# Optimization experiments

Measured on AMD Instinct MI355X. Metric: run time of the kernel, lower is better.

The kernel has to match this reference:

```python
import jax, jax.numpy as jnp
import numpy as np

B, L, E = 2, 8192, 1024
H, D = 16, 64          # num_heads, head_dim (E = H*D)
C = 256                # chunk_size
EPS = 1e-6
LN_EPS = 1e-5


def setup_inputs() -> dict:
    key = jax.random.key(0)
    ks = jax.random.split(key, 12)
    w = lambda k, shape: (jax.random.normal(k, shape, jnp.float32) * 0.02)
    return {
        "x": jax.random.normal(ks[0], (B, L, E), jnp.float32),
        "Wq": w(ks[1], (E, E)), "bq": jnp.zeros((E,), jnp.float32),
        "Wk": w(ks[2], (E, E)), "bk": jnp.zeros((E,), jnp.float32),
        "Wv": w(ks[3], (E, E)), "bv": jnp.zeros((E,), jnp.float32),
        "Wo": w(ks[4], (E, E)), "bo": jnp.zeros((E,), jnp.float32),
        "gamma": jnp.ones((E,), jnp.float32),
        "beta": jnp.zeros((E,), jnp.float32),
    }


def _split_heads(t):
    # [B, L, E] -> [B, H, L, D]
    return t.reshape(B, L, H, D).transpose(0, 2, 1, 3)


def _phi(x):
    # feature map: elu(x) + 1  (strictly positive)
    return jax.nn.elu(x) + 1.0


def _chunkwise_linear_attention(q, k, v):
    """Causal linear attention via chunkwise parallel scan.

    q, k, v: [B, H, L, D] (q, k already feature-mapped, positive).
    out[t] = q_t @ S_t / (q_t . z_t), S_t = sum_{s<=t} k_s v_s^T, z_t = sum_{s<=t} k_s.
    """
    N = L // C
    # [N, B, H, C, D]
    qc = q.reshape(B, H, N, C, D).transpose(2, 0, 1, 3, 4)
    kc = k.reshape(B, H, N, C, D).transpose(2, 0, 1, 3, 4)
    vc = v.reshape(B, H, N, C, D).transpose(2, 0, 1, 3, 4)
    mask = jnp.tril(jnp.ones((C, C), q.dtype))  # causal within chunk (inclusive)

    def step(carry, inp):
        S, z = carry                      # S: [B,H,D,D], z: [B,H,D]
        qi, ki, vi = inp                  # [B,H,C,D]
        scores = jnp.einsum("bhcd,bhed->bhce", qi, ki) * mask  # [B,H,C,C]
        num = jnp.einsum("bhcd,bhde->bhce", qi, S) \
            + jnp.einsum("bhce,bhed->bhcd", scores, vi)
        den = jnp.einsum("bhcd,bhd->bhc", qi, z) + scores.sum(-1)
        out = num / (den + EPS)[..., None]
        S = S + jnp.einsum("bhcd,bhce->bhde", ki, vi)
        z = z + ki.sum(axis=2)
        return (S, z), out

    S0 = jnp.zeros((B, H, D, D), q.dtype)
    z0 = jnp.zeros((B, H, D), q.dtype)
    _, outs = jax.lax.scan(step, (S0, z0), (qc, kc, vc))
    # [N,B,H,C,D] -> [B,H,L,D]
    return outs.transpose(1, 2, 0, 3, 4).reshape(B, H, L, D)


def _layer_norm(x, gamma, beta):
    mu = x.mean(-1, keepdims=True)
    var = ((x - mu) ** 2).mean(-1, keepdims=True)
    return gamma * (x - mu) * jax.lax.rsqrt(var + LN_EPS) + beta


def reference(x, Wq, bq, Wk, bk, Wv, bv, Wo, bo, gamma, beta):
    residual = x
    q = _phi(_split_heads(x @ Wq + bq))
    k = _phi(_split_heads(x @ Wk + bk))
    v = _split_heads(x @ Wv + bv)
    out = _chunkwise_linear_attention(q, k, v)      # [B,H,L,D]
    out = out.transpose(0, 2, 1, 3).reshape(B, L, E)
    out = out @ Wo + bo
    return _layer_norm(out + residual, gamma, beta)
```

## Files before the change

### kernel.cpp

```cpp
#include <hip/hip_runtime.h>
#include <stdint.h>

typedef __attribute__((ext_vector_type(8))) short bf16x8;
typedef __attribute__((ext_vector_type(4))) float f32x4;
typedef __attribute__((ext_vector_type(2))) unsigned int u32x2;
typedef unsigned short u16;
typedef unsigned int u32;

#define MFMA16(a, b, c) __builtin_amdgcn_mfma_f32_16x16x32_bf16((a), (b), (c), 0, 0, 0)

__device__ __forceinline__ u16 f2bf(float f) {
  union { float f; u32 u; } c; c.f = f;
  u32 u = c.u;
  return (u16)((u + 0x7FFFu + ((u >> 16) & 1u)) >> 16);
}

__device__ __forceinline__ float bf2f(u16 h) {
  union { u32 u; float f; } c;
  c.u = ((u32)h) << 16;
  return c.f;
}

__device__ __forceinline__ void gll16(const void* g, void* l) {
  __builtin_amdgcn_global_load_lds((__attribute__((address_space(1))) void*)(g),
                                   (__attribute__((address_space(3))) void*)(l),
                                   16, 0, 0);
}

__global__ __launch_bounds__(256) void cast_k(const float* __restrict__ x, u16* __restrict__ xb) {
  int idx = blockIdx.x * 256 + threadIdx.x;
#pragma unroll
  for (int it = 0; it < 4; it++) {
    size_t i = (size_t)idx + (size_t)it * 1048576;
    float4 v = ((const float4*)x)[i];
    u32x2 p;
    p.x = (u32)f2bf(v.x) | ((u32)f2bf(v.y) << 16);
    p.y = (u32)f2bf(v.z) | ((u32)f2bf(v.w) << 16);
    ((u32x2*)xb)[i] = p;
  }
}

__global__ __launch_bounds__(256) void wT_k(const float* __restrict__ Wq, const float* __restrict__ Wk,
                                            const float* __restrict__ Wv, const float* __restrict__ Wo,
                                            u16* __restrict__ wqkvT, u16* __restrict__ woT) {
  __shared__ float t[32][33];
  int which = blockIdx.z;
  const float* W = (which == 0) ? Wq : (which == 1) ? Wk : (which == 2) ? Wv : Wo;
  int k0 = blockIdx.y * 32, n0 = blockIdx.x * 32;
  int c = threadIdx.x & 31, r8 = threadIdx.x >> 5;
#pragma unroll
  for (int rr = 0; rr < 32; rr += 8)
    t[r8 + rr][c] = W[(size_t)(k0 + r8 + rr) * 1024 + n0 + c];
  __syncthreads();
  u16* outp = (which < 3) ? (wqkvT + (size_t)which * 1048576) : woT;
#pragma unroll
  for (int rr = 0; rr < 32; rr += 8)
    outp[(size_t)(n0 + r8 + rr) * 1024 + k0 + c] = f2bf(t[c][r8 + rr]);
}

template <int MODE>
__global__ __launch_bounds__(256, 2) void gemm_k(
    const u16* __restrict__ A, const u16* __restrict__ Bt,
    const float* __restrict__ b0, const float* __restrict__ b1, const float* __restrict__ b2,
    u16* __restrict__ q_o, u16* __restrict__ k_o, u16* __restrict__ vt_o,
    const u16* __restrict__ xres, u16* __restrict__ y_o) {
  __shared__ u16 As[2][4096];
  __shared__ u16 Bs[2][4096];
  const int tid = threadIdx.x;
  const int wave = tid >> 6, lane = tid & 63;
  const int quad = lane >> 4, l16 = lane & 15;
  const int wr = wave >> 1, wc = wave & 1;
  const int bm = blockIdx.x, bn = blockIdx.y;

  const int r_a = wave * 32 + (lane >> 2);
  const int c_a = (lane & 3) * 8;
  const size_t arow = (size_t)bm * 128;
  const size_t brow = (size_t)bn * 128;

  f32x4 zero = {0.f, 0.f, 0.f, 0.f};
  f32x4 acc[4][4];
#pragma unroll
  for (int i = 0; i < 4; i++)
#pragma unroll
    for (int j = 0; j < 4; j++) acc[i][j] = zero;

  for (int k0 = 0; k0 < 1024; k0 += 64) {
#pragma unroll
    for (int h = 0; h < 2; h++) {
      const int kk = k0 + h * 32;
#pragma unroll
      for (int jc = 0; jc < 2; jc++) {
        int r = r_a + jc * 16;
        int lo = wave * 1024 + jc * 512 + lane * 8;
        gll16(A + (arow + r) * 1024 + kk + c_a, &As[h][lo]);
        gll16(Bt + (brow + r) * 1024 + kk + c_a, &Bs[h][lo]);
      }
    }
    __syncthreads();
#pragma unroll
    for (int h = 0; h < 2; h++) {
      bf16x8 af[4], bf[4];
#pragma unroll
      for (int t = 0; t < 4; t++) af[t] = *(const bf16x8*)&As[h][(wr * 64 + t * 16 + l16) * 32 + quad * 8];
#pragma unroll
      for (int t = 0; t < 4; t++) bf[t] = *(const bf16x8*)&Bs[h][(wc * 64 + t * 16 + l16) * 32 + quad * 8];
#pragma unroll
      for (int i = 0; i < 4; i++)
#pragma unroll
        for (int j = 0; j < 4; j++) acc[i][j] = MFMA16(af[i], bf[j], acc[i][j]);
    }
    __syncthreads();
  }

  if (MODE == 0) {
#pragma unroll
    for (int i = 0; i < 4; i++) {
      const int m0 = bm * 128 + wr * 64 + i * 16 + quad * 4;
      const int b = m0 >> 13, l0 = m0 & 8191;
      const int nch = l0 >> 8, c0 = l0 & 255;
#pragma unroll
      for (int j = 0; j < 4; j++) {
        const int n_g = bn * 128 + wc * 64 + j * 16 + l16;
        const int sec = n_g >> 10, e = n_g & 1023;
        const float* bias = (sec == 0) ? b0 : ((sec == 1) ? b1 : b2);
        const float be = bias[e];
        float v4[4];
#pragma unroll
        for (int r = 0; r < 4; r++) {
          float v = acc[i][j][r] + be;
          if (sec < 2) v = (v > 0.f) ? (v + 1.f) : __expf(v);
          v4[r] = v;
        }
        const int h = e >> 6, d = e & 63;
        const int bh = b * 16 + h;
        if (sec == 2) {
          u32x2 p;
          p.x = (u32)f2bf(v4[0]) | ((u32)f2bf(v4[1]) << 16);
          p.y = (u32)f2bf(v4[2]) | ((u32)f2bf(v4[3]) << 16);
          *(u32x2*)&vt_o[(((size_t)(bh * 32 + nch)) * 64 + d) * 256 + c0] = p;
        } else {
          u16* dst = (sec == 0) ? q_o : k_o;
          const size_t tb = (((size_t)bh * 8192 + l0) << 6) + d;
#pragma unroll
          for (int r = 0; r < 4; r++) dst[tb + (size_t)r * 64] = f2bf(v4[r]);
        }
      }
    }
  } else {
#pragma unroll
    for (int i = 0; i < 4; i++) {
#pragma unroll
      for (int j = 0; j < 4; j++) {
#pragma unroll
        for (int r = 0; r < 4; r++) {
          int m_g = bm * 128 + wr * 64 + i * 16 + quad * 4 + r;
          int n_g = bn * 128 + wc * 64 + j * 16 + l16;
          float v = acc[i][j][r] + b0[n_g] + bf2f(xres[(size_t)m_g * 1024 + n_g]);
          y_o[(size_t)m_g * 1024 + n_g] = f2bf(v);
        }
      }
    }
  }
}

__global__ __launch_bounds__(256, 2) void phaseA_k(const u16* __restrict__ kb, const u16* __restrict__ vt,
                                                   float* __restrict__ ST, float* __restrict__ zc) {
  __shared__ u16 kT[64 * 264];
  const int tid = threadIdx.x;
  const int wave = tid >> 6, lane = tid & 63;
  const int quad = lane >> 4, l16 = lane & 15;
  const int wr = wave >> 1, wc = wave & 1;
  const int bhn = blockIdx.x;
  const u16* kc = kb + (size_t)bhn * 16384;
  const u16* vtc = vt + (size_t)bhn * 16384;

#pragma unroll
  for (int t = 0; t < 2; t++) {
    const int dblk = wave + 4 * t;
#pragma unroll
    for (int itc = 0; itc < 4; itc++) {
      const int c = itc * 64 + lane;
      bf16x8 kv = *(const bf16x8*)&kc[c * 64 + dblk * 8];
#pragma unroll
      for (int j = 0; j < 8; j++) kT[(dblk * 8 + j) * 264 + c] = (u16)kv[j];
    }
  }
  __syncthreads();

  f32x4 zero = {0.f, 0.f, 0.f, 0.f};
  f32x4 t4[2][2];
  f32x4 za[2];
#pragma unroll
  for (int i = 0; i < 2; i++) {
    za[i] = zero;
#pragma unroll
    for (int j = 0; j < 2; j++) t4[i][j] = zero;
  }
  bf16x8 ones;
#pragma unroll
  for (int j = 0; j < 8; j++) ones[j] = (short)0x3F80;

#pragma unroll
  for (int ks = 0; ks < 8; ks++) {
    bf16x8 av[2], bk2[2];
#pragma unroll
    for (int t = 0; t < 2; t++) av[t] = *(const bf16x8*)&vtc[(wr * 32 + t * 16 + l16) * 256 + ks * 32 + quad * 8];
#pragma unroll
    for (int t = 0; t < 2; t++) bk2[t] = *(const bf16x8*)&kT[(wc * 32 + t * 16 + l16) * 264 + ks * 32 + quad * 8];
#pragma unroll
    for (int i = 0; i < 2; i++)
#pragma unroll
      for (int j = 0; j < 2; j++) t4[i][j] = MFMA16(av[i], bk2[j], t4[i][j]);
    if (wr == 0) {
#pragma unroll
      for (int j = 0; j < 2; j++) za[j] = MFMA16(ones, bk2[j], za[j]);
    }
  }
  float* Sg = ST + (size_t)bhn * 4096;
#pragma unroll
  for (int i = 0; i < 2; i++)
#pragma unroll
    for (int j = 0; j < 2; j++)
#pragma unroll
      for (int r = 0; r < 4; r++)
        Sg[(wr * 32 + i * 16 + quad * 4 + r) * 64 + wc * 32 + j * 16 + l16] = t4[i][j][r];
  if (wr == 0 && quad == 0) {
#pragma unroll
    for (int j = 0; j < 2; j++) zc[(size_t)bhn * 64 + wc * 32 + j * 16 + l16] = za[j][0];
  }
}

__global__ __launch_bounds__(256) void phaseB_k(const float* __restrict__ ST, const float* __restrict__ zc,
                                                u16* __restrict__ STp, u16* __restrict__ zp) {
  const int blk = blockIdx.x, tid = threadIdx.x;
  if (blk < 512) {
    const int bh = blk >> 4;
    const int e = ((blk & 15) << 8) + tid;
    const size_t base = (size_t)bh * 32 * 4096 + e;
    float run = 0.f;
#pragma unroll
    for (int n = 0; n < 32; n++) {
      float v = ST[base + (size_t)n * 4096];
      STp[base + (size_t)n * 4096] = f2bf(run);
      run += v;
    }
  } else {
    const int idx = (blk - 512) * 256 + tid;
    const int bh = idx >> 6, d = idx & 63;
    const size_t zb = (size_t)bh * 2048 + d;
    float run = 0.f;
#pragma unroll
    for (int n = 0; n < 32; n++) {
      float v = zc[zb + n * 64];
      zp[zb + n * 64] = f2bf(run);
      run += v;
    }
  }
}

__global__ __launch_bounds__(256, 2) void phaseC_k(const u16* __restrict__ qb, const u16* __restrict__ kb,
                                                   const u16* __restrict__ vt, const u16* __restrict__ STp,
                                                   const u16* __restrict__ zp, u16* __restrict__ ao) {
  __shared__ u16 P[4][64 * 72];
  const int tid = threadIdx.x;
  const int wave = tid >> 6, lane = tid & 63;
  const int quad = lane >> 4, l16 = lane & 15;
  const int bhn = blockIdx.x;
  const int bh = bhn >> 5, n = bhn & 31;
  const int b = bh >> 4, h = bh & 15;
  const size_t cbase = (size_t)bhn * 16384;
  const u16* qc = qb + cbase;
  const u16* kc = kb + cbase;
  const u16* vtc = vt + cbase;
  const u16* STg = STp + (size_t)bhn * 4096;
  const u16* zg = zp + (size_t)bhn * 64;

  f32x4 zero = {0.f, 0.f, 0.f, 0.f};
  f32x4 num[4][4];
  f32x4 den[4];
#pragma unroll
  for (int i = 0; i < 4; i++) {
    den[i] = zero;
#pragma unroll
    for (int j = 0; j < 4; j++) num[i][j] = zero;
  }
  bf16x8 ones;
#pragma unroll
  for (int j = 0; j < 8; j++) ones[j] = (short)0x3F80;

  bf16x8 aq[4][2];
#pragma unroll
  for (int i = 0; i < 4; i++)
#pragma unroll
    for (int ks = 0; ks < 2; ks++)
      aq[i][ks] = *(const bf16x8*)&qc[(wave * 64 + i * 16 + l16) * 64 + ks * 32 + quad * 8];

#pragma unroll
  for (int ks = 0; ks < 2; ks++) {
    bf16x8 bz = *(const bf16x8*)&zg[ks * 32 + quad * 8];
    bf16x8 bs[4];
#pragma unroll
    for (int j = 0; j < 4; j++) bs[j] = *(const bf16x8*)&STg[(j * 16 + l16) * 64 + ks * 32 + quad * 8];
#pragma unroll
    for (int i = 0; i < 4; i++) {
      den[i] = MFMA16(aq[i][ks], bz, den[i]);
#pragma unroll
      for (int j = 0; j < 4; j++) num[i][j] = MFMA16(aq[i][ks], bs[j], num[i][j]);
    }
  }

  u16* Pw = &P[wave][0];

  for (int cc = 0; cc <= wave; cc++) {
    bf16x8 bkf[2][4];
#pragma unroll
    for (int ks = 0; ks < 2; ks++)
#pragma unroll
      for (int j = 0; j < 4; j++)
        bkf[ks][j] = *(const bf16x8*)&kc[(cc * 64 + j * 16 + l16) * 64 + ks * 32 + quad * 8];
#pragma unroll
    for (int i = 0; i < 4; i++) {
      f32x4 sc4[4];
#pragma unroll
      for (int j = 0; j < 4; j++) sc4[j] = zero;
#pragma unroll
      for (int ks = 0; ks < 2; ks++)
#pragma unroll
        for (int j = 0; j < 4; j++) sc4[j] = MFMA16(aq[i][ks], bkf[ks][j], sc4[j]);
#pragma unroll
      for (int j = 0; j < 4; j++) {
#pragma unroll
        for (int r = 0; r < 4; r++) {
          int row = wave * 64 + i * 16 + quad * 4 + r;
          int col = cc * 64 + j * 16 + l16;
          float v = (col <= row) ? sc4[j][r] : 0.f;
          Pw[(i * 16 + quad * 4 + r) * 72 + j * 16 + l16] = f2bf(v);
        }
      }
    }
    bf16x8 bvf[2][4];
#pragma unroll
    for (int ks2 = 0; ks2 < 2; ks2++)
#pragma unroll
      for (int j = 0; j < 4; j++)
        bvf[ks2][j] = *(const bf16x8*)&vtc[(j * 16 + l16) * 256 + cc * 64 + ks2 * 32 + quad * 8];
#pragma unroll
    for (int i = 0; i < 4; i++) {
#pragma unroll
      for (int ks2 = 0; ks2 < 2; ks2++) {
        bf16x8 ap = *(const bf16x8*)&Pw[(i * 16 + l16) * 72 + ks2 * 32 + quad * 8];
#pragma unroll
        for (int j = 0; j < 4; j++) num[i][j] = MFMA16(ap, bvf[ks2][j], num[i][j]);
        den[i] = MFMA16(ap, ones, den[i]);
      }
    }
  }

#pragma unroll
  for (int i = 0; i < 4; i++)
#pragma unroll
    for (int j = 0; j < 4; j++)
#pragma unroll
      for (int r = 0; r < 4; r++) {
        int row = wave * 64 + i * 16 + quad * 4 + r;
        int col = j * 16 + l16;
        float o = num[i][j][r] / (den[i][r] + 1e-6f);
        int l = n * 256 + row;
        ao[(((size_t)b * 8192 + l) * 16 + h) * 64 + col] = f2bf(o);
      }
}

__global__ __launch_bounds__(256) void ln_k(const u16* __restrict__ y, const float* __restrict__ gamma,
                                            const float* __restrict__ beta, float* __restrict__ o) {
  int row = blockIdx.x, tid = threadIdx.x;
  u32x2 pv = ((const u32x2*)(y + (size_t)row * 1024))[tid];
  float vx = bf2f((u16)(pv.x & 0xFFFF)), vy = bf2f((u16)(pv.x >> 16));
  float vz = bf2f((u16)(pv.y & 0xFFFF)), vw = bf2f((u16)(pv.y >> 16));
  float s = vx + vy + vz + vw;
  float s2 = vx * vx + vy * vy + vz * vz + vw * vw;
#pragma unroll
  for (int off = 32; off; off >>= 1) {
    s += __shfl_down(s, off, 64);
    s2 += __shfl_down(s2, off, 64);
  }
  __shared__ float red[8];
  int wave = tid >> 6, lane = tid & 63;
  if (lane == 0) { red[wave] = s; red[4 + wave] = s2; }
  __syncthreads();
  s = red[0] + red[1] + red[2] + red[3];
  s2 = red[4] + red[5] + red[6] + red[7];
  float mu = s * 0.0009765625f;
  float var = s2 * 0.0009765625f - mu * mu;
  float inv = rsqrtf(var + 1e-5f);
  float4 g = ((const float4*)gamma)[tid];
  float4 bb = ((const float4*)beta)[tid];
  float4 ov;
  ov.x = g.x * (vx - mu) * inv + bb.x;
  ov.y = g.y * (vy - mu) * inv + bb.y;
  ov.z = g.z * (vz - mu) * inv + bb.z;
  ov.w = g.w * (vw - mu) * inv + bb.w;
  ((float4*)(o + (size_t)row * 1024))[tid] = ov;
}

extern "C" void kernel_launch(void* const* d_in, const int* in_sizes, int n_in,
                              void* d_out, int out_size, void* d_ws, size_t ws_size,
                              hipStream_t stream) {
  const float* x = (const float*)d_in[0];
  const float* Wq = (const float*)d_in[1];
  const float* bq = (const float*)d_in[2];
  const float* Wk = (const float*)d_in[3];
  const float* bk = (const float*)d_in[4];
  const float* Wv = (const float*)d_in[5];
  const float* bv = (const float*)d_in[6];
  const float* Wo = (const float*)d_in[7];
  const float* bo = (const float*)d_in[8];
  const float* gamma = (const float*)d_in[9];
  const float* beta = (const float*)d_in[10];

  char* ws = (char*)d_ws;
  u16* xb = (u16*)(ws + 0);
  u16* qb = (u16*)(ws + 33554432);
  u16* kb = (u16*)(ws + 67108864);
  u16* attno = (u16*)(ws + 100663296);
  u16* vt = (u16*)(ws + 134217728);
  u16* wqkvT = (u16*)(ws + 167772160);
  u16* woT = (u16*)(ws + 174063616);
  float* SchT = (float*)(ws + 176160768);
  float* zch = (float*)(ws + 192937984);
  u16* STp = (u16*)(ws + 193200128);
  u16* zp = (u16*)(ws + 201588736);
  u16* ypre = qb;

  cast_k<<<4096, 256, 0, stream>>>(x, xb);
  wT_k<<<dim3(32, 32, 4), 256, 0, stream>>>(Wq, Wk, Wv, Wo, wqkvT, woT);
  gemm_k<0><<<dim3(128, 24), 256, 0, stream>>>(xb, wqkvT, bq, bk, bv, qb, kb, vt, nullptr, nullptr);
  phaseA_k<<<1024, 256, 0, stream>>>(kb, vt, SchT, zch);
  phaseB_k<<<520, 256, 0, stream>>>(SchT, zch, STp, zp);
  phaseC_k<<<1024, 256, 0, stream>>>(qb, kb, vt, STp, zp, attno);
  gemm_k<1><<<dim3(128, 8), 256, 0, stream>>>(attno, woT, bo, nullptr, nullptr, nullptr, nullptr, nullptr, xb,
                                              ypre);
  ln_k<<<16384, 256, 0, stream>>>(ypre, gamma, beta, (float*)d_out);
}
```

Baseline: 389.4 us.

## Merge prep kernels, swap GEMM grid order, store chunk states in bf16

```diff
diff --git a/kernel.cpp b/kernel.cpp
--- a/kernel.cpp
+++ b/kernel.cpp
@@ -27,39 +27,42 @@
                                    16, 0, 0);
 }
 
-__global__ __launch_bounds__(256) void cast_k(const float* __restrict__ x, u16* __restrict__ xb) {
-  int idx = blockIdx.x * 256 + threadIdx.x;
-#pragma unroll
-  for (int it = 0; it < 4; it++) {
-    size_t i = (size_t)idx + (size_t)it * 1048576;
-    float4 v = ((const float4*)x)[i];
-    u32x2 p;
-    p.x = (u32)f2bf(v.x) | ((u32)f2bf(v.y) << 16);
-    p.y = (u32)f2bf(v.z) | ((u32)f2bf(v.w) << 16);
-    ((u32x2*)xb)[i] = p;
-  }
-}
-
-__global__ __launch_bounds__(256) void wT_k(const float* __restrict__ Wq, const float* __restrict__ Wk,
-                                            const float* __restrict__ Wv, const float* __restrict__ Wo,
-                                            u16* __restrict__ wqkvT, u16* __restrict__ woT) {
-  __shared__ float t[32][33];
-  int which = blockIdx.z;
-  const float* W = (which == 0) ? Wq : (which == 1) ? Wk : (which == 2) ? Wv : Wo;
-  int k0 = blockIdx.y * 32, n0 = blockIdx.x * 32;
-  int c = threadIdx.x & 31, r8 = threadIdx.x >> 5;
-#pragma unroll
-  for (int rr = 0; rr < 32; rr += 8)
-    t[r8 + rr][c] = W[(size_t)(k0 + r8 + rr) * 1024 + n0 + c];
-  __syncthreads();
-  u16* outp = (which < 3) ? (wqkvT + (size_t)which * 1048576) : woT;
-#pragma unroll
-  for (int rr = 0; rr < 32; rr += 8)
-    outp[(size_t)(n0 + r8 + rr) * 1024 + k0 + c] = f2bf(t[c][r8 + rr]);
+__global__ __launch_bounds__(256) void prep_k(const float* __restrict__ x, u16* __restrict__ xb,
+                                              const float* __restrict__ Wq, const float* __restrict__ Wk,
+                                              const float* __restrict__ Wv, const float* __restrict__ Wo,
+                                              u16* __restrict__ wqkvT, u16* __restrict__ woT) {
+  const int blk = blockIdx.x;
+  if (blk < 4096) {
+    int idx = blk * 256 + threadIdx.x;
+#pragma unroll
+    for (int it = 0; it < 4; it++) {
+      size_t i = (size_t)idx + (size_t)it * 1048576;
+      float4 v = ((const float4*)x)[i];
+      u32x2 p;
+      p.x = (u32)f2bf(v.x) | ((u32)f2bf(v.y) << 16);
+      p.y = (u32)f2bf(v.z) | ((u32)f2bf(v.w) << 16);
+      ((u32x2*)xb)[i] = p;
+    }
+  } else {
+    __shared__ float t[32][33];
+    const int id = blk - 4096;
+    const int which = id >> 10, rem = id & 1023;
+    const float* W = (which == 0) ? Wq : (which == 1) ? Wk : (which == 2) ? Wv : Wo;
+    int k0 = (rem >> 5) * 32, n0 = (rem & 31) * 32;
+    int c = threadIdx.x & 31, r8 = threadIdx.x >> 5;
+#pragma unroll
+    for (int rr = 0; rr < 32; rr += 8)
+      t[r8 + rr][c] = W[(size_t)(k0 + r8 + rr) * 1024 + n0 + c];
+    __syncthreads();
+    u16* outp = (which < 3) ? (wqkvT + (size_t)which * 1048576) : woT;
+#pragma unroll
+    for (int rr = 0; rr < 32; rr += 8)
+      outp[(size_t)(n0 + r8 + rr) * 1024 + k0 + c] = f2bf(t[c][r8 + rr]);
+  }
 }
 
 template <int MODE>
-__global__ __launch_bounds__(256, 2) void gemm_k(
+__global__ __launch_bounds__(256, 4) void gemm_k(
     const u16* __restrict__ A, const u16* __restrict__ Bt,
     const float* __restrict__ b0, const float* __restrict__ b1, const float* __restrict__ b2,
     u16* __restrict__ q_o, u16* __restrict__ k_o, u16* __restrict__ vt_o,
@@ -70,7 +73,7 @@
   const int wave = tid >> 6, lane = tid & 63;
   const int quad = lane >> 4, l16 = lane & 15;
   const int wr = wave >> 1, wc = wave & 1;
-  const int bm = blockIdx.x, bn = blockIdx.y;
+  const int bn = blockIdx.x, bm = blockIdx.y;
 
   const int r_a = wave * 32 + (lane >> 2);
   const int c_a = (lane & 3) * 8;
@@ -164,7 +167,7 @@
 }
 
 __global__ __launch_bounds__(256, 2) void phaseA_k(const u16* __restrict__ kb, const u16* __restrict__ vt,
-                                                   float* __restrict__ ST, float* __restrict__ zc) {
+                                                   u16* __restrict__ Sch, u16* __restrict__ zc) {
   __shared__ u16 kT[64 * 264];
   const int tid = threadIdx.x;
   const int wave = tid >> 6, lane = tid & 63;
@@ -216,21 +219,21 @@
       for (int j = 0; j < 2; j++) za[j] = MFMA16(ones, bk2[j], za[j]);
     }
   }
-  float* Sg = ST + (size_t)bhn * 4096;
+  u16* Sg = Sch + (size_t)bhn * 4096;
 #pragma unroll
   for (int i = 0; i < 2; i++)
 #pragma unroll
     for (int j = 0; j < 2; j++)
 #pragma unroll
       for (int r = 0; r < 4; r++)
-        Sg[(wr * 32 + i * 16 + quad * 4 + r) * 64 + wc * 32 + j * 16 + l16] = t4[i][j][r];
+        Sg[(wr * 32 + i * 16 + quad * 4 + r) * 64 + wc * 32 + j * 16 + l16] = f2bf(t4[i][j][r]);
   if (wr == 0 && quad == 0) {
 #pragma unroll
-    for (int j = 0; j < 2; j++) zc[(size_t)bhn * 64 + wc * 32 + j * 16 + l16] = za[j][0];
-  }
-}
-
-__global__ __launch_bounds__(256) void phaseB_k(const float* __restrict__ ST, const float* __restrict__ zc,
+    for (int j = 0; j < 2; j++) zc[(size_t)bhn * 64 + wc * 32 + j * 16 + l16] = f2bf(za[j][0]);
+  }
+}
+
+__global__ __launch_bounds__(256) void phaseB_k(const u16* __restrict__ Sch, const u16* __restrict__ zc,
                                                 u16* __restrict__ STp, u16* __restrict__ zp) {
   const int blk = blockIdx.x, tid = threadIdx.x;
   if (blk < 512) {
@@ -240,7 +243,7 @@
     float run = 0.f;
 #pragma unroll
     for (int n = 0; n < 32; n++) {
-      float v = ST[base + (size_t)n * 4096];
+      float v = bf2f(Sch[base + (size_t)n * 4096]);
       STp[base + (size_t)n * 4096] = f2bf(run);
       run += v;
     }
@@ -251,7 +254,7 @@
     float run = 0.f;
 #pragma unroll
     for (int n = 0; n < 32; n++) {
-      float v = zc[zb + n * 64];
+      float v = bf2f(zc[zb + n * 64]);
       zp[zb + n * 64] = f2bf(run);
       run += v;
     }
@@ -425,19 +428,18 @@
   u16* vt = (u16*)(ws + 134217728);
   u16* wqkvT = (u16*)(ws + 167772160);
   u16* woT = (u16*)(ws + 174063616);
-  float* SchT = (float*)(ws + 176160768);
-  float* zch = (float*)(ws + 192937984);
-  u16* STp = (u16*)(ws + 193200128);
-  u16* zp = (u16*)(ws + 201588736);
+  u16* Sch = (u16*)(ws + 176160768);
+  u16* zch = (u16*)(ws + 184549376);
+  u16* STp = (u16*)(ws + 184680448);
+  u16* zp = (u16*)(ws + 193069056);
   u16* ypre = qb;
 
-  cast_k<<<4096, 256, 0, stream>>>(x, xb);
-  wT_k<<<dim3(32, 32, 4), 256, 0, stream>>>(Wq, Wk, Wv, Wo, wqkvT, woT);
-  gemm_k<0><<<dim3(128, 24), 256, 0, stream>>>(xb, wqkvT, bq, bk, bv, qb, kb, vt, nullptr, nullptr);
-  phaseA_k<<<1024, 256, 0, stream>>>(kb, vt, SchT, zch);
-  phaseB_k<<<520, 256, 0, stream>>>(SchT, zch, STp, zp);
+  prep_k<<<8192, 256, 0, stream>>>(x, xb, Wq, Wk, Wv, Wo, wqkvT, woT);
+  gemm_k<0><<<dim3(24, 128), 256, 0, stream>>>(xb, wqkvT, bq, bk, bv, qb, kb, vt, nullptr, nullptr);
+  phaseA_k<<<1024, 256, 0, stream>>>(kb, vt, Sch, zch);
+  phaseB_k<<<520, 256, 0, stream>>>(Sch, zch, STp, zp);
   phaseC_k<<<1024, 256, 0, stream>>>(qb, kb, vt, STp, zp, attno);
-  gemm_k<1><<<dim3(128, 8), 256, 0, stream>>>(attno, woT, bo, nullptr, nullptr, nullptr, nullptr, nullptr, xb,
+  gemm_k<1><<<dim3(8, 128), 256, 0, stream>>>(attno, woT, bo, nullptr, nullptr, nullptr, nullptr, nullptr, xb,
                                               ypre);
   ln_k<<<16384, 256, 0, stream>>>(ypre, gamma, beta, (float*)d_out);
 }
```

After: 392.4 us. No clear change (+0.8%).
